# Optimization experiments

Measured on AMD Instinct MI355X. Metric: run time of the kernel, lower is better.

## Reference

```python
import jax, jax.numpy as jnp
import numpy as np

B, N = 8, 2048
IN_DIM, MEM_DIM, CTX_DIM = 256, 256, 128

def _linear_params(key, out_dim, in_dim):
    kw, kb = jax.random.split(key)
    bound = 1.0 / np.sqrt(in_dim)
    W = jax.random.uniform(kw, (out_dim, in_dim), jnp.float32, -bound, bound)
    b = jax.random.uniform(kb, (out_dim,), jnp.float32, -bound, bound)
    return W, b

def setup_inputs() -> dict:
    key = jax.random.key(0)
    ks = jax.random.split(key, 8)
    Wq, bq = _linear_params(ks[0], CTX_DIM, IN_DIM)
    Wk, bk = _linear_params(ks[1], CTX_DIM, MEM_DIM)
    Wv, bv = _linear_params(ks[2], MEM_DIM, MEM_DIM)
    Wu, bu = _linear_params(ks[3], MEM_DIM, IN_DIM + MEM_DIM)
    Wr, br = _linear_params(ks[4], MEM_DIM, IN_DIM + MEM_DIM)
    Wc, bc = _linear_params(ks[5], MEM_DIM, IN_DIM + MEM_DIM)
    input_tensor = jax.random.normal(ks[6], (B, N, IN_DIM), jnp.float32)
    previous_memory = jax.random.normal(ks[7], (B, N, MEM_DIM), jnp.float32)
    return dict(input_tensor=input_tensor, previous_memory=previous_memory,
                Wq=Wq, bq=bq, Wk=Wk, bk=bk, Wv=Wv, bv=bv,
                Wu=Wu, bu=bu, Wr=Wr, br=br, Wc=Wc, bc=bc)

def reference(input_tensor, previous_memory, Wq, bq, Wk, bk, Wv, bv, Wu, bu, Wr, br, Wc, bc):
    # QKV projections (torch Linear: y = x @ W.T + b)
    query = jnp.einsum('bnd,cd->bnc', input_tensor, Wq) + bq        # [B,N,CTX]
    key = jnp.einsum('bnm,cm->bnc', previous_memory, Wk) + bk       # [B,N,CTX]
    value = jnp.einsum('bnm,vm->bnv', previous_memory, Wv) + bv     # [B,N,MEM]
    attention_scores = jnp.einsum('bqc,bkc->bqk', query, key)        # [B,N,N]
    attention_probs = jax.nn.softmax(attention_scores, axis=-1)
    context_vector = jnp.einsum('bqk,bkv->bqv', attention_probs, value)  # computed but unused downstream, as in original
    combined = jnp.concatenate([input_tensor, previous_memory], axis=-1)  # [B,N,IN+MEM]
    update_gate = jax.nn.sigmoid(jnp.einsum('bnd,md->bnm', combined, Wu) + bu)
    reset_gate = jax.nn.sigmoid(jnp.einsum('bnd,md->bnm', combined, Wr) + br)
    cand_in = jnp.concatenate([input_tensor, reset_gate * previous_memory], axis=-1)
    candidate_memory = jnp.tanh(jnp.einsum('bnd,md->bnm', cand_in, Wc) + bc)
    new_memory = (1.0 - update_gate) * previous_memory + update_gate * candidate_memory
    return new_memory, attention_probs
```

## Files before the change

### kernel.cpp

```cpp
#include <hip/hip_runtime.h>


typedef _Float16 half8 __attribute__((ext_vector_type(8)));
typedef _Float16 half4 __attribute__((ext_vector_type(4)));
typedef float floatx4 __attribute__((ext_vector_type(4)));

#define MFMA16(a, b, c) __builtin_amdgcn_mfma_f32_16x16x32_f16((a), (b), (c), 0, 0, 0)

#define OFF_Q   524288
#define OFF_K   2621440

__device__ __forceinline__ void gload16(const void* g, void* l) {
  __builtin_amdgcn_global_load_lds((const __attribute__((address_space(1))) unsigned int*)g,
                                   (__attribute__((address_space(3))) unsigned int*)l, 16, 0, 0);
}

__global__ __launch_bounds__(512, 4) void kA(
    const float* __restrict__ input, const float* __restrict__ prev,
    const float* __restrict__ Wq, const float* __restrict__ bq,
    const float* __restrict__ Wk, const float* __restrict__ bk,
    const float* __restrict__ Wr, const float* __restrict__ br,
    const float* __restrict__ Wu, const float* __restrict__ bu,
    _Float16* __restrict__ ws,
    _Float16* __restrict__ t_sc, _Float16* __restrict__ u_sc)
{
  __shared__ char smem[32768];
  const int tid = threadIdx.x, w = tid >> 6, l = tid & 63;
  const int lr = l & 15, lg = l >> 4;

  if (blockIdx.x < 512) {
    const int b2 = blockIdx.x;
    const int rows0 = (b2 & 127) * 128;
    const int isU = w >> 2;
    const int c = (b2 >> 7) * 64 + (w & 3) * 16 + lr;

    const float* Wf = isU ? Wu : Wr;
    half8 bw[16];
#pragma unroll
    for (int ks = 0; ks < 16; ++ks) {
      floatx4 w0 = *(const floatx4*)(Wf + (size_t)c * 512 + ks * 32 + lg * 8);
      floatx4 w1 = *(const floatx4*)(Wf + (size_t)c * 512 + ks * 32 + lg * 8 + 4);
      half8 h;
#pragma unroll
      for (int j = 0; j < 4; ++j) { h[j] = (_Float16)w0[j]; h[4 + j] = (_Float16)w1[j]; }
      bw[ks] = h;
    }
    const float bv = (isU ? bu : br)[c];

    const int srow = tid >> 5, scol = (tid & 31) * 8;
    const int ssz = (srow & 7) << 4;
    floatx4 sI0, sI1, sP0, sP1;

#define K2RU_LOAD(ch) { \
  const float* si = input + ((size_t)rows0 + (ch) * 16 + srow) * 256 + scol; \
  const float* sp = prev  + ((size_t)rows0 + (ch) * 16 + srow) * 256 + scol; \
  sI0 = *(const floatx4*)si; sI1 = *(const floatx4*)(si + 4); \
  sP0 = *(const floatx4*)sp; sP1 = *(const floatx4*)(sp + 4); }
#define K2RU_WRITE(ch) { char* bufw = smem + ((ch) & 1) * 16384; \
  half8 hi, hp; \
  _Pragma("unroll") for (int j = 0; j < 4; ++j) { \
    hi[j] = (_Float16)sI0[j]; hi[4+j] = (_Float16)sI1[j]; \
    hp[j] = (_Float16)sP0[j]; hp[4+j] = (_Float16)sP1[j]; } \
  int o = srow * 1024 + ((scol * 2) ^ ssz); \
  *(half8*)(bufw + o) = hi; *(half8*)(bufw + o + 512) = hp; }

    K2RU_LOAD(0); K2RU_WRITE(0);
    __syncthreads();
#pragma unroll 1
    for (int ch = 0; ch < 8; ++ch) {
      if (ch < 7) K2RU_LOAD(ch + 1);
      const char* buf = smem + (ch & 1) * 16384;
      floatx4 acc = {0.f, 0.f, 0.f, 0.f};
      const int base = lr * 1024, sz = (lr & 7) << 4;
#pragma unroll
      for (int ks = 0; ks < 16; ++ks) {
        half8 a = *(const half8*)(buf + base + ((ks * 64 + lg * 16) ^ sz));
        acc = MFMA16(a, bw[ks], acc);
      }
#pragma unroll
      for (int j = 0; j < 4; ++j) {
        const int crow = lg * 4 + j;
        const size_t grow = (size_t)rows0 + ch * 16 + crow;
        float g = 1.f / (1.f + __expf(-(acc[j] + bv)));
        if (!isU) {
          float m = (float)*(const _Float16*)(buf + crow * 1024 + 512 + ((c * 2) ^ ((crow & 7) << 4)));
          t_sc[grow * 256 + c] = (_Float16)(g * m);
        } else {
          u_sc[grow * 256 + c] = (_Float16)g;
        }
      }
      if (ch < 7) K2RU_WRITE(ch + 1);
      __syncthreads();
    }
  } else {
    const int b1 = blockIdx.x - 512;
    const int which = b1 >> 8;
    const int rows0 = (b1 & 255) * 64;
    const float* x = which ? prev : input;
    const float* Wf = which ? Wk : Wq;
    const float* bias = which ? bk : bq;
    _Float16* out = ws + (which ? OFF_K : OFF_Q);
    const int c = w * 16 + lr;

    half8 bh[8], blo[8];
#pragma unroll
    for (int ks = 0; ks < 8; ++ks) {
      floatx4 w0 = *(const floatx4*)(Wf + (size_t)c * 256 + ks * 32 + lg * 8);
      floatx4 w1 = *(const floatx4*)(Wf + (size_t)c * 256 + ks * 32 + lg * 8 + 4);
      half8 h, lo;
#pragma unroll
      for (int j = 0; j < 4; ++j) {
        _Float16 h0 = (_Float16)w0[j];
        h[j] = h0; lo[j] = (_Float16)(w0[j] - (float)h0);
        _Float16 h1 = (_Float16)w1[j];
        h[4 + j] = h1; lo[4 + j] = (_Float16)(w1[j] - (float)h1);
      }
      bh[ks] = h; blo[ks] = lo;
    }
    const float bv = bias[c];

    const int srow = tid >> 5, scol = (tid & 31) * 8;
    const int ssz = (srow & 7) << 4;
    floatx4 st0, st1;

#define K1_LOAD(ch) { const float* src = x + ((size_t)rows0 + (ch) * 16 + srow) * 256 + scol; \
  st0 = *(const floatx4*)src; st1 = *(const floatx4*)(src + 4); }
#define K1_WRITE(ch) { char* bufw = smem + ((ch) & 1) * 8192; \
  half8 h; \
  _Pragma("unroll") for (int j = 0; j < 4; ++j) { \
    h[j] = (_Float16)st0[j]; h[4+j] = (_Float16)st1[j]; } \
  *(half8*)(bufw + srow * 512 + ((scol * 2) ^ ssz)) = h; }

    K1_LOAD(0); K1_WRITE(0);
    __syncthreads();
#pragma unroll 1
    for (int ch = 0; ch < 4; ++ch) {
      if (ch < 3) K1_LOAD(ch + 1);
      const char* buf = smem + (ch & 1) * 8192;
      floatx4 acc = {0.f, 0.f, 0.f, 0.f};
      const int base = lr * 512, sz = (lr & 7) << 4;
#pragma unroll
      for (int ks = 0; ks < 8; ++ks) {
        half8 ah = *(const half8*)(buf + base + ((ks * 64 + lg * 16) ^ sz));
        acc = MFMA16(ah, bh[ks], acc);
        acc = MFMA16(ah, blo[ks], acc);
      }
#pragma unroll
      for (int j = 0; j < 4; ++j)
        out[((size_t)rows0 + ch * 16 + lg * 4 + j) * 128 + c] = (_Float16)(acc[j] + bv);
      if (ch < 3) K1_WRITE(ch + 1);
      __syncthreads();
    }
  }
}

#define K3_STAGE(Kg, dst, ch) { \
  const char* g_ = (Kg) + (ch) * 32768; \
  _Pragma("unroll") for (int i_ = 0; i_ < 4; ++i_) { \
    int o_ = w * 1024 + i_ * 8192 + l * 16; \
    int row_ = o_ >> 8, col_ = o_ & 255; \
    gload16(g_ + row_ * 256 + (col_ ^ ((row_ & 7) << 4)), (dst) + w * 1024 + i_ * 8192); } }

__global__ __launch_bounds__(512, 4) void kB(
    const float* __restrict__ input, const float* __restrict__ prev,
    const float* __restrict__ Wc, const float* __restrict__ bc,
    const _Float16* __restrict__ ws, float* __restrict__ part,
    const _Float16* __restrict__ t_sc, const _Float16* __restrict__ u_sc,
    float* __restrict__ out0)
{
  __shared__ char smem[65536];
  const int tid = threadIdx.x, w = tid >> 6, l = tid & 63;
  const int lr = l & 15, lg = l >> 4;

  if (blockIdx.x < 512) {
    const int b3 = blockIdx.x;
    const int b = b3 & 7, q0 = ((b3 >> 3) & 15) * 128, kh = b3 >> 7;

    const _Float16* Q = ws + OFF_Q + ((size_t)b * 2048 + q0 + w * 16) * 128;
    const char* Kg = (const char*)(ws + OFF_K + ((size_t)b * 2048 + kh * 512) * 128);

    half8 qf[4];
#pragma unroll
    for (int ks = 0; ks < 4; ++ks)
      qf[ks] = *(const half8*)(Q + (size_t)lr * 128 + ks * 32 + lg * 8);

    char* kbuf0 = smem, * kbuf1 = smem + 32768;
    K3_STAGE(Kg, kbuf0, 0);
    __syncthreads();

    float se = 0.f;
#pragma unroll 1
    for (int ch = 0; ch < 4; ++ch) {
      if (ch < 3) K3_STAGE(Kg, ((ch + 1) & 1) ? kbuf1 : kbuf0, ch + 1);
      const char* buf = (ch & 1) ? kbuf1 : kbuf0;
#pragma unroll
      for (int kt = 0; kt < 8; ++kt) {
        const int kk = kt * 16 + lr;
        const int kbase = kk * 256, ksz = (kk & 7) << 4;
        half8 kf[4];
#pragma unroll
        for (int ks = 0; ks < 4; ++ks)
          kf[ks] = *(const half8*)(buf + kbase + ((ks * 64 + lg * 16) ^ ksz));
        floatx4 acc = {0.f, 0.f, 0.f, 0.f};
#pragma unroll
        for (int ks = 0; ks < 4; ++ks) acc = MFMA16(kf[ks], qf[ks], acc);
#pragma unroll
        for (int j = 0; j < 4; ++j) se += __expf(acc[j] - 14.f);
      }
      __syncthreads();
    }
    se += __shfl_xor(se, 16);
    se += __shfl_xor(se, 32);
    if (lg == 0)
      part[((size_t)b * 4 + kh) * 2048 + q0 + w * 16 + lr] = se;
  } else {
    const int b2 = blockIdx.x - 512;
    const int rows0 = (b2 & 255) * 64;
    const int c = (b2 >> 8) * 128 + w * 16 + lr;

    half8 bw[16];
#pragma unroll
    for (int ks = 0; ks < 16; ++ks) {
      floatx4 w0 = *(const floatx4*)(Wc + (size_t)c * 512 + ks * 32 + lg * 8);
      floatx4 w1 = *(const floatx4*)(Wc + (size_t)c * 512 + ks * 32 + lg * 8 + 4);
      half8 h;
#pragma unroll
      for (int j = 0; j < 4; ++j) { h[j] = (_Float16)w0[j]; h[4 + j] = (_Float16)w1[j]; }
      bw[ks] = h;
    }
    const float bv = bc[c];

    const int srow = tid >> 5, scol = (tid & 31) * 8;
    const int ssz = (srow & 7) << 4;
    floatx4 sI0, sI1;
    half8 sT;

#define K2C_LOAD(ch) { \
  const float* si = input + ((size_t)rows0 + (ch) * 16 + srow) * 256 + scol; \
  sI0 = *(const floatx4*)si; sI1 = *(const floatx4*)(si + 4); \
  sT = *(const half8*)(t_sc + ((size_t)rows0 + (ch) * 16 + srow) * 256 + scol); }
#define K2C_WRITE(ch) { char* bufw = smem + ((ch) & 1) * 16384; \
  half8 hi; \
  _Pragma("unroll") for (int j = 0; j < 4; ++j) { hi[j] = (_Float16)sI0[j]; hi[4+j] = (_Float16)sI1[j]; } \
  int o = srow * 1024 + ((scol * 2) ^ ssz); \
  *(half8*)(bufw + o) = hi; *(half8*)(bufw + o + 512) = sT; }

    K2C_LOAD(0); K2C_WRITE(0);
    __syncthreads();
#pragma unroll 1
    for (int ch = 0; ch < 4; ++ch) {
      if (ch < 3) K2C_LOAD(ch + 1);
      const char* buf = smem + (ch & 1) * 16384;
      floatx4 acc = {0.f, 0.f, 0.f, 0.f};
      const int base = lr * 1024, sz = (lr & 7) << 4;
#pragma unroll
      for (int ks = 0; ks < 16; ++ks) {
        half8 a = *(const half8*)(buf + base + ((ks * 64 + lg * 16) ^ sz));
        acc = MFMA16(a, bw[ks], acc);
      }
#pragma unroll
      for (int j = 0; j < 4; ++j) {
        const size_t grow = (size_t)rows0 + ch * 16 + lg * 4 + j;
        float e2 = __expf(2.f * (acc[j] + bv));
        float cg = (e2 - 1.f) / (e2 + 1.f);
        float u = (float)u_sc[grow * 256 + c];
        float m = prev[grow * 256 + c];
        out0[grow * 256 + c] = (1.f - u) * m + u * cg;
      }
      if (ch < 3) K2C_WRITE(ch + 1);
      __syncthreads();
    }
  }
}

__global__ __launch_bounds__(512) void k3b_store(
    const _Float16* __restrict__ ws, const float* __restrict__ part,
    float* __restrict__ out1)
{
  __shared__ char kbuf[2][32768];
  const int b = blockIdx.x, q0 = blockIdx.y * 128, kh = blockIdx.z;
  const int tid = threadIdx.x, w = tid >> 6, l = tid & 63;
  const int lr = l & 15, lg = l >> 4;

  const int q = q0 + w * 16 + lr;
  const _Float16* Q = ws + OFF_Q + ((size_t)b * 2048 + q0 + w * 16) * 128;
  const char* Kg = (const char*)(ws + OFF_K + ((size_t)b * 2048 + kh * 512) * 128);

  half8 qf[4];
#pragma unroll
  for (int ks = 0; ks < 4; ++ks)
    qf[ks] = *(const half8*)(Q + (size_t)lr * 128 + ks * 32 + lg * 8);
  const float inv = 1.f / (part[(size_t)(b * 4 + 0) * 2048 + q] +
                           part[(size_t)(b * 4 + 1) * 2048 + q] +
                           part[(size_t)(b * 4 + 2) * 2048 + q] +
                           part[(size_t)(b * 4 + 3) * 2048 + q]);

  K3_STAGE(Kg, kbuf[0], 0);
  __syncthreads();

  float* orow = out1 + ((size_t)b * 2048 + q) * 2048 + kh * 512;
#pragma unroll 1
  for (int ch = 0; ch < 4; ++ch) {
    if (ch < 3) K3_STAGE(Kg, kbuf[(ch + 1) & 1], ch + 1);
    const char* buf = kbuf[ch & 1];
#pragma unroll
    for (int kt = 0; kt < 8; ++kt) {
      const int kk = kt * 16 + lr;
      const int kbase = kk * 256, ksz = (kk & 7) << 4;
      half8 kf[4];
#pragma unroll
      for (int ks = 0; ks < 4; ++ks)
        kf[ks] = *(const half8*)(buf + kbase + ((ks * 64 + lg * 16) ^ ksz));
      floatx4 acc = {0.f, 0.f, 0.f, 0.f};
#pragma unroll
      for (int ks = 0; ks < 4; ++ks) acc = MFMA16(kf[ks], qf[ks], acc);
      floatx4 v;
#pragma unroll
      for (int j = 0; j < 4; ++j) v[j] = __expf(acc[j] - 14.f) * inv;
      *(floatx4*)(orow + ch * 128 + kt * 16 + lg * 4) = v;
    }
    __syncthreads();
  }
}

extern "C" void kernel_launch(void* const* d_in, const int* in_sizes, int n_in,
                              void* d_out, int out_size, void* d_ws, size_t ws_size,
                              hipStream_t stream)
{
  const float* input = (const float*)d_in[0];
  const float* prev  = (const float*)d_in[1];
  const float* Wq = (const float*)d_in[2];
  const float* bq = (const float*)d_in[3];
  const float* Wk = (const float*)d_in[4];
  const float* bk = (const float*)d_in[5];
  const float* Wu = (const float*)d_in[8];
  const float* bu = (const float*)d_in[9];
  const float* Wr = (const float*)d_in[10];
  const float* br = (const float*)d_in[11];
  const float* Wc = (const float*)d_in[12];
  const float* bc = (const float*)d_in[13];

  float* out0 = (float*)d_out;
  float* out1 = out0 + (size_t)8 * 2048 * 256;
  _Float16* ws = (_Float16*)d_ws;

  _Float16* t_sc = (_Float16*)out1;
  _Float16* u_sc = (_Float16*)out1 + 4194304;
  float* part = (float*)ws;

  hipLaunchKernelGGL(kA, dim3(1024), dim3(512), 0, stream,
                     input, prev, Wq, bq, Wk, bk, Wr, br, Wu, bu, ws, t_sc, u_sc);
  hipLaunchKernelGGL(kB, dim3(1024), dim3(512), 0, stream,
                     input, prev, Wc, bc, ws, part, t_sc, u_sc, out0);
  hipLaunchKernelGGL(k3b_store, dim3(8, 16, 4), dim3(512), 0, stream, ws, part, out1);
}
```

Before: 110.3 us.

## Fuse three kernels into one cooperative persistent kernel with grid barriers

Moves each former kernel's work into a device role function and runs all of them from one cooperative kernel of 512 blocks. Each block runs two roles in sequence (gates plus QK projection, then softmax sums plus candidate update, then the probability store), and grid.sync separates the phases. The aim is to cut kernel launch and tail gaps between the three launches. In exchange each block does serial work, grid barriers add their own cost, and an occupancy query runs on every call; the old three-kernel path is kept as a fallback when fewer than two blocks fit per CU.

```diff
diff --git a/kernel.cpp b/kernel.cpp
--- a/kernel.cpp
+++ b/kernel.cpp
@@ -1,4 +1,7 @@
 #include <hip/hip_runtime.h>
+#include <hip/hip_cooperative_groups.h>
+
+namespace cg = cooperative_groups;
 
 
 typedef _Float16 half8 __attribute__((ext_vector_type(8)));
@@ -15,41 +18,36 @@
                                    (__attribute__((address_space(3))) unsigned int*)l, 16, 0, 0);
 }
 
-__global__ __launch_bounds__(512, 4) void kA(
-    const float* __restrict__ input, const float* __restrict__ prev,
-    const float* __restrict__ Wq, const float* __restrict__ bq,
-    const float* __restrict__ Wk, const float* __restrict__ bk,
+
+__device__ __forceinline__ void role_k2ru(
+    char* smem, int job, int tid,
+    const float* __restrict__ input, const float* __restrict__ prev,
     const float* __restrict__ Wr, const float* __restrict__ br,
     const float* __restrict__ Wu, const float* __restrict__ bu,
-    _Float16* __restrict__ ws,
     _Float16* __restrict__ t_sc, _Float16* __restrict__ u_sc)
 {
-  __shared__ char smem[32768];
-  const int tid = threadIdx.x, w = tid >> 6, l = tid & 63;
+  const int w = tid >> 6, l = tid & 63;
   const int lr = l & 15, lg = l >> 4;
-
-  if (blockIdx.x < 512) {
-    const int b2 = blockIdx.x;
-    const int rows0 = (b2 & 127) * 128;
-    const int isU = w >> 2;
-    const int c = (b2 >> 7) * 64 + (w & 3) * 16 + lr;
-
-    const float* Wf = isU ? Wu : Wr;
-    half8 bw[16];
-#pragma unroll
-    for (int ks = 0; ks < 16; ++ks) {
-      floatx4 w0 = *(const floatx4*)(Wf + (size_t)c * 512 + ks * 32 + lg * 8);
-      floatx4 w1 = *(const floatx4*)(Wf + (size_t)c * 512 + ks * 32 + lg * 8 + 4);
-      half8 h;
-#pragma unroll
-      for (int j = 0; j < 4; ++j) { h[j] = (_Float16)w0[j]; h[4 + j] = (_Float16)w1[j]; }
-      bw[ks] = h;
-    }
-    const float bv = (isU ? bu : br)[c];
-
-    const int srow = tid >> 5, scol = (tid & 31) * 8;
-    const int ssz = (srow & 7) << 4;
-    floatx4 sI0, sI1, sP0, sP1;
+  const int rows0 = (job & 127) * 128;
+  const int isU = w >> 2;
+  const int c = (job >> 7) * 64 + (w & 3) * 16 + lr;
+
+  const float* Wf = isU ? Wu : Wr;
+  half8 bw[16];
+#pragma unroll
+  for (int ks = 0; ks < 16; ++ks) {
+    floatx4 w0 = *(const floatx4*)(Wf + (size_t)c * 512 + ks * 32 + lg * 8);
+    floatx4 w1 = *(const floatx4*)(Wf + (size_t)c * 512 + ks * 32 + lg * 8 + 4);
+    half8 h;
+#pragma unroll
+    for (int j = 0; j < 4; ++j) { h[j] = (_Float16)w0[j]; h[4 + j] = (_Float16)w1[j]; }
+    bw[ks] = h;
+  }
+  const float bv = (isU ? bu : br)[c];
+
+  const int srow = tid >> 5, scol = (tid & 31) * 8;
+  const int ssz = (srow & 7) << 4;
+  floatx4 sI0, sI1, sP0, sP1;
 
 #define K2RU_LOAD(ch) { \
   const float* si = input + ((size_t)rows0 + (ch) * 16 + srow) * 256 + scol; \
@@ -64,64 +62,73 @@
   int o = srow * 1024 + ((scol * 2) ^ ssz); \
   *(half8*)(bufw + o) = hi; *(half8*)(bufw + o + 512) = hp; }
 
-    K2RU_LOAD(0); K2RU_WRITE(0);
+  K2RU_LOAD(0); K2RU_WRITE(0);
+  __syncthreads();
+#pragma unroll 1
+  for (int ch = 0; ch < 8; ++ch) {
+    if (ch < 7) K2RU_LOAD(ch + 1);
+    const char* buf = smem + (ch & 1) * 16384;
+    floatx4 acc = {0.f, 0.f, 0.f, 0.f};
+    const int base = lr * 1024, sz = (lr & 7) << 4;
+#pragma unroll
+    for (int ks = 0; ks < 16; ++ks) {
+      half8 a = *(const half8*)(buf + base + ((ks * 64 + lg * 16) ^ sz));
+      acc = MFMA16(a, bw[ks], acc);
+    }
+#pragma unroll
+    for (int j = 0; j < 4; ++j) {
+      const int crow = lg * 4 + j;
+      const size_t grow = (size_t)rows0 + ch * 16 + crow;
+      float g = 1.f / (1.f + __expf(-(acc[j] + bv)));
+      if (!isU) {
+        float m = (float)*(const _Float16*)(buf + crow * 1024 + 512 + ((c * 2) ^ ((crow & 7) << 4)));
+        t_sc[grow * 256 + c] = (_Float16)(g * m);
+      } else {
+        u_sc[grow * 256 + c] = (_Float16)g;
+      }
+    }
+    if (ch < 7) K2RU_WRITE(ch + 1);
     __syncthreads();
-#pragma unroll 1
-    for (int ch = 0; ch < 8; ++ch) {
-      if (ch < 7) K2RU_LOAD(ch + 1);
-      const char* buf = smem + (ch & 1) * 16384;
-      floatx4 acc = {0.f, 0.f, 0.f, 0.f};
-      const int base = lr * 1024, sz = (lr & 7) << 4;
-#pragma unroll
-      for (int ks = 0; ks < 16; ++ks) {
-        half8 a = *(const half8*)(buf + base + ((ks * 64 + lg * 16) ^ sz));
-        acc = MFMA16(a, bw[ks], acc);
-      }
-#pragma unroll
-      for (int j = 0; j < 4; ++j) {
-        const int crow = lg * 4 + j;
-        const size_t grow = (size_t)rows0 + ch * 16 + crow;
-        float g = 1.f / (1.f + __expf(-(acc[j] + bv)));
-        if (!isU) {
-          float m = (float)*(const _Float16*)(buf + crow * 1024 + 512 + ((c * 2) ^ ((crow & 7) << 4)));
-          t_sc[grow * 256 + c] = (_Float16)(g * m);
-        } else {
-          u_sc[grow * 256 + c] = (_Float16)g;
-        }
-      }
-      if (ch < 7) K2RU_WRITE(ch + 1);
-      __syncthreads();
-    }
-  } else {
-    const int b1 = blockIdx.x - 512;
-    const int which = b1 >> 8;
-    const int rows0 = (b1 & 255) * 64;
-    const float* x = which ? prev : input;
-    const float* Wf = which ? Wk : Wq;
-    const float* bias = which ? bk : bq;
-    _Float16* out = ws + (which ? OFF_K : OFF_Q);
-    const int c = w * 16 + lr;
-
-    half8 bh[8], blo[8];
-#pragma unroll
-    for (int ks = 0; ks < 8; ++ks) {
-      floatx4 w0 = *(const floatx4*)(Wf + (size_t)c * 256 + ks * 32 + lg * 8);
-      floatx4 w1 = *(const floatx4*)(Wf + (size_t)c * 256 + ks * 32 + lg * 8 + 4);
-      half8 h, lo;
-#pragma unroll
-      for (int j = 0; j < 4; ++j) {
-        _Float16 h0 = (_Float16)w0[j];
-        h[j] = h0; lo[j] = (_Float16)(w0[j] - (float)h0);
-        _Float16 h1 = (_Float16)w1[j];
-        h[4 + j] = h1; lo[4 + j] = (_Float16)(w1[j] - (float)h1);
-      }
-      bh[ks] = h; blo[ks] = lo;
-    }
-    const float bv = bias[c];
-
-    const int srow = tid >> 5, scol = (tid & 31) * 8;
-    const int ssz = (srow & 7) << 4;
-    floatx4 st0, st1;
+  }
+}
+
+__device__ __forceinline__ void role_k1(
+    char* smem, int job, int tid,
+    const float* __restrict__ input, const float* __restrict__ prev,
+    const float* __restrict__ Wq, const float* __restrict__ bq,
+    const float* __restrict__ Wk, const float* __restrict__ bk,
+    _Float16* __restrict__ ws)
+{
+  const int w = tid >> 6, l = tid & 63;
+  const int lr = l & 15, lg = l >> 4;
+  const int which = job >> 8;
+  const int rows0 = (job & 255) * 64;
+  const float* x = which ? prev : input;
+  const float* Wf = which ? Wk : Wq;
+  const float* bias = which ? bk : bq;
+  _Float16* out = ws + (which ? OFF_K : OFF_Q);
+  const int c = w * 16 + lr;
+
+  half8 bh[8], blo[8];
+#pragma unroll
+  for (int ks = 0; ks < 8; ++ks) {
+    floatx4 w0 = *(const floatx4*)(Wf + (size_t)c * 256 + ks * 32 + lg * 8);
+    floatx4 w1 = *(const floatx4*)(Wf + (size_t)c * 256 + ks * 32 + lg * 8 + 4);
+    half8 h, lo;
+#pragma unroll
+    for (int j = 0; j < 4; ++j) {
+      _Float16 h0 = (_Float16)w0[j];
+      h[j] = h0; lo[j] = (_Float16)(w0[j] - (float)h0);
+      _Float16 h1 = (_Float16)w1[j];
+      h[4 + j] = h1; lo[4 + j] = (_Float16)(w1[j] - (float)h1);
+    }
+    bh[ks] = h; blo[ks] = lo;
+  }
+  const float bv = bias[c];
+
+  const int srow = tid >> 5, scol = (tid & 31) * 8;
+  const int ssz = (srow & 7) << 4;
+  floatx4 st0, st1;
 
 #define K1_LOAD(ch) { const float* src = x + ((size_t)rows0 + (ch) * 16 + srow) * 256 + scol; \
   st0 = *(const floatx4*)src; st1 = *(const floatx4*)(src + 4); }
@@ -131,26 +138,25 @@
     h[j] = (_Float16)st0[j]; h[4+j] = (_Float16)st1[j]; } \
   *(half8*)(bufw + srow * 512 + ((scol * 2) ^ ssz)) = h; }
 
-    K1_LOAD(0); K1_WRITE(0);
+  K1_LOAD(0); K1_WRITE(0);
+  __syncthreads();
+#pragma unroll 1
+  for (int ch = 0; ch < 4; ++ch) {
+    if (ch < 3) K1_LOAD(ch + 1);
+    const char* buf = smem + (ch & 1) * 8192;
+    floatx4 acc = {0.f, 0.f, 0.f, 0.f};
+    const int base = lr * 512, sz = (lr & 7) << 4;
+#pragma unroll
+    for (int ks = 0; ks < 8; ++ks) {
+      half8 ah = *(const half8*)(buf + base + ((ks * 64 + lg * 16) ^ sz));
+      acc = MFMA16(ah, bh[ks], acc);
+      acc = MFMA16(ah, blo[ks], acc);
+    }
+#pragma unroll
+    for (int j = 0; j < 4; ++j)
+      out[((size_t)rows0 + ch * 16 + lg * 4 + j) * 128 + c] = (_Float16)(acc[j] + bv);
+    if (ch < 3) K1_WRITE(ch + 1);
     __syncthreads();
-#pragma unroll 1
-    for (int ch = 0; ch < 4; ++ch) {
-      if (ch < 3) K1_LOAD(ch + 1);
-      const char* buf = smem + (ch & 1) * 8192;
-      floatx4 acc = {0.f, 0.f, 0.f, 0.f};
-      const int base = lr * 512, sz = (lr & 7) << 4;
-#pragma unroll
-      for (int ks = 0; ks < 8; ++ks) {
-        half8 ah = *(const half8*)(buf + base + ((ks * 64 + lg * 16) ^ sz));
-        acc = MFMA16(ah, bh[ks], acc);
-        acc = MFMA16(ah, blo[ks], acc);
-      }
-#pragma unroll
-      for (int j = 0; j < 4; ++j)
-        out[((size_t)rows0 + ch * 16 + lg * 4 + j) * 128 + c] = (_Float16)(acc[j] + bv);
-      if (ch < 3) K1_WRITE(ch + 1);
-      __syncthreads();
-    }
   }
 }
 
@@ -161,79 +167,81 @@
     int row_ = o_ >> 8, col_ = o_ & 255; \
     gload16(g_ + row_ * 256 + (col_ ^ ((row_ & 7) << 4)), (dst) + w * 1024 + i_ * 8192); } }
 
-__global__ __launch_bounds__(512, 4) void kB(
+__device__ __forceinline__ void role_k3a(
+    char* smem, int job, int tid,
+    const _Float16* __restrict__ ws, float* __restrict__ part)
+{
+  const int w = tid >> 6, l = tid & 63;
+  const int lr = l & 15, lg = l >> 4;
+  const int b = job & 7, q0 = ((job >> 3) & 15) * 128, kh = job >> 7;
+
+  const _Float16* Q = ws + OFF_Q + ((size_t)b * 2048 + q0 + w * 16) * 128;
+  const char* Kg = (const char*)(ws + OFF_K + ((size_t)b * 2048 + kh * 512) * 128);
+
+  half8 qf[4];
+#pragma unroll
+  for (int ks = 0; ks < 4; ++ks)
+    qf[ks] = *(const half8*)(Q + (size_t)lr * 128 + ks * 32 + lg * 8);
+
+  char* kbuf0 = smem; char* kbuf1 = smem + 32768;
+  K3_STAGE(Kg, kbuf0, 0);
+  __syncthreads();
+
+  float se = 0.f;
+#pragma unroll 1
+  for (int ch = 0; ch < 4; ++ch) {
+    if (ch < 3) K3_STAGE(Kg, ((ch + 1) & 1) ? kbuf1 : kbuf0, ch + 1);
+    const char* buf = (ch & 1) ? kbuf1 : kbuf0;
+#pragma unroll
+    for (int kt = 0; kt < 8; ++kt) {
+      const int kk = kt * 16 + lr;
+      const int kbase = kk * 256, ksz = (kk & 7) << 4;
+      half8 kf[4];
+#pragma unroll
+      for (int ks = 0; ks < 4; ++ks)
+        kf[ks] = *(const half8*)(buf + kbase + ((ks * 64 + lg * 16) ^ ksz));
+      floatx4 acc = {0.f, 0.f, 0.f, 0.f};
+#pragma unroll
+      for (int ks = 0; ks < 4; ++ks) acc = MFMA16(kf[ks], qf[ks], acc);
+#pragma unroll
+      for (int j = 0; j < 4; ++j) se += __expf(acc[j] - 14.f);
+    }
+    __syncthreads();
+  }
+  se += __shfl_xor(se, 16);
+  se += __shfl_xor(se, 32);
+  if (lg == 0)
+    part[((size_t)b * 4 + kh) * 2048 + q0 + w * 16 + lr] = se;
+}
+
+__device__ __forceinline__ void role_k2c(
+    char* smem, int job, int tid,
     const float* __restrict__ input, const float* __restrict__ prev,
     const float* __restrict__ Wc, const float* __restrict__ bc,
-    const _Float16* __restrict__ ws, float* __restrict__ part,
     const _Float16* __restrict__ t_sc, const _Float16* __restrict__ u_sc,
     float* __restrict__ out0)
 {
-  __shared__ char smem[65536];
-  const int tid = threadIdx.x, w = tid >> 6, l = tid & 63;
+  const int w = tid >> 6, l = tid & 63;
   const int lr = l & 15, lg = l >> 4;
-
-  if (blockIdx.x < 512) {
-    const int b3 = blockIdx.x;
-    const int b = b3 & 7, q0 = ((b3 >> 3) & 15) * 128, kh = b3 >> 7;
-
-    const _Float16* Q = ws + OFF_Q + ((size_t)b * 2048 + q0 + w * 16) * 128;
-    const char* Kg = (const char*)(ws + OFF_K + ((size_t)b * 2048 + kh * 512) * 128);
-
-    half8 qf[4];
-#pragma unroll
-    for (int ks = 0; ks < 4; ++ks)
-      qf[ks] = *(const half8*)(Q + (size_t)lr * 128 + ks * 32 + lg * 8);
-
-    char* kbuf0 = smem, * kbuf1 = smem + 32768;
-    K3_STAGE(Kg, kbuf0, 0);
-    __syncthreads();
-
-    float se = 0.f;
-#pragma unroll 1
-    for (int ch = 0; ch < 4; ++ch) {
-      if (ch < 3) K3_STAGE(Kg, ((ch + 1) & 1) ? kbuf1 : kbuf0, ch + 1);
-      const char* buf = (ch & 1) ? kbuf1 : kbuf0;
-#pragma unroll
-      for (int kt = 0; kt < 8; ++kt) {
-        const int kk = kt * 16 + lr;
-        const int kbase = kk * 256, ksz = (kk & 7) << 4;
-        half8 kf[4];
-#pragma unroll
-        for (int ks = 0; ks < 4; ++ks)
-          kf[ks] = *(const half8*)(buf + kbase + ((ks * 64 + lg * 16) ^ ksz));
-        floatx4 acc = {0.f, 0.f, 0.f, 0.f};
-#pragma unroll
-        for (int ks = 0; ks < 4; ++ks) acc = MFMA16(kf[ks], qf[ks], acc);
-#pragma unroll
-        for (int j = 0; j < 4; ++j) se += __expf(acc[j] - 14.f);
-      }
-      __syncthreads();
-    }
-    se += __shfl_xor(se, 16);
-    se += __shfl_xor(se, 32);
-    if (lg == 0)
-      part[((size_t)b * 4 + kh) * 2048 + q0 + w * 16 + lr] = se;
-  } else {
-    const int b2 = blockIdx.x - 512;
-    const int rows0 = (b2 & 255) * 64;
-    const int c = (b2 >> 8) * 128 + w * 16 + lr;
-
-    half8 bw[16];
-#pragma unroll
-    for (int ks = 0; ks < 16; ++ks) {
-      floatx4 w0 = *(const floatx4*)(Wc + (size_t)c * 512 + ks * 32 + lg * 8);
-      floatx4 w1 = *(const floatx4*)(Wc + (size_t)c * 512 + ks * 32 + lg * 8 + 4);
-      half8 h;
-#pragma unroll
-      for (int j = 0; j < 4; ++j) { h[j] = (_Float16)w0[j]; h[4 + j] = (_Float16)w1[j]; }
-      bw[ks] = h;
-    }
-    const float bv = bc[c];
-
-    const int srow = tid >> 5, scol = (tid & 31) * 8;
-    const int ssz = (srow & 7) << 4;
-    floatx4 sI0, sI1;
-    half8 sT;
+  const int rows0 = (job & 255) * 64;
+  const int c = (job >> 8) * 128 + w * 16 + lr;
+
+  half8 bw[16];
+#pragma unroll
+  for (int ks = 0; ks < 16; ++ks) {
+    floatx4 w0 = *(const floatx4*)(Wc + (size_t)c * 512 + ks * 32 + lg * 8);
+    floatx4 w1 = *(const floatx4*)(Wc + (size_t)c * 512 + ks * 32 + lg * 8 + 4);
+    half8 h;
+#pragma unroll
+    for (int j = 0; j < 4; ++j) { h[j] = (_Float16)w0[j]; h[4 + j] = (_Float16)w1[j]; }
+    bw[ks] = h;
+  }
+  const float bv = bc[c];
+
+  const int srow = tid >> 5, scol = (tid & 31) * 8;
+  const int ssz = (srow & 7) << 4;
+  floatx4 sI0, sI1;
+  half8 sT;
 
 #define K2C_LOAD(ch) { \
   const float* si = input + ((size_t)rows0 + (ch) * 16 + srow) * 256 + scol; \
@@ -245,42 +253,41 @@
   int o = srow * 1024 + ((scol * 2) ^ ssz); \
   *(half8*)(bufw + o) = hi; *(half8*)(bufw + o + 512) = sT; }
 
-    K2C_LOAD(0); K2C_WRITE(0);
+  K2C_LOAD(0); K2C_WRITE(0);
+  __syncthreads();
+#pragma unroll 1
+  for (int ch = 0; ch < 4; ++ch) {
+    if (ch < 3) K2C_LOAD(ch + 1);
+    const char* buf = smem + (ch & 1) * 16384;
+    floatx4 acc = {0.f, 0.f, 0.f, 0.f};
+    const int base = lr * 1024, sz = (lr & 7) << 4;
+#pragma unroll
+    for (int ks = 0; ks < 16; ++ks) {
+      half8 a = *(const half8*)(buf + base + ((ks * 64 + lg * 16) ^ sz));
+      acc = MFMA16(a, bw[ks], acc);
+    }
+#pragma unroll
+    for (int j = 0; j < 4; ++j) {
+      const size_t grow = (size_t)rows0 + ch * 16 + lg * 4 + j;
+      float e2 = __expf(2.f * (acc[j] + bv));
+      float cg = (e2 - 1.f) / (e2 + 1.f);
+      float u = (float)u_sc[grow * 256 + c];
+      float m = prev[grow * 256 + c];
+      out0[grow * 256 + c] = (1.f - u) * m + u * cg;
+    }
+    if (ch < 3) K2C_WRITE(ch + 1);
     __syncthreads();
-#pragma unroll 1
-    for (int ch = 0; ch < 4; ++ch) {
-      if (ch < 3) K2C_LOAD(ch + 1);
-      const char* buf = smem + (ch & 1) * 16384;
-      floatx4 acc = {0.f, 0.f, 0.f, 0.f};
-      const int base = lr * 1024, sz = (lr & 7) << 4;
-#pragma unroll
-      for (int ks = 0; ks < 16; ++ks) {
-        half8 a = *(const half8*)(buf + base + ((ks * 64 + lg * 16) ^ sz));
-        acc = MFMA16(a, bw[ks], acc);
-      }
-#pragma unroll
-      for (int j = 0; j < 4; ++j) {
-        const size_t grow = (size_t)rows0 + ch * 16 + lg * 4 + j;
-        float e2 = __expf(2.f * (acc[j] + bv));
-        float cg = (e2 - 1.f) / (e2 + 1.f);
-        float u = (float)u_sc[grow * 256 + c];
-        float m = prev[grow * 256 + c];
-        out0[grow * 256 + c] = (1.f - u) * m + u * cg;
-      }
-      if (ch < 3) K2C_WRITE(ch + 1);
-      __syncthreads();
-    }
-  }
-}
-
-__global__ __launch_bounds__(512) void k3b_store(
+  }
+}
+
+__device__ __forceinline__ void role_k3b(
+    char* smem, int job, int tid,
     const _Float16* __restrict__ ws, const float* __restrict__ part,
     float* __restrict__ out1)
 {
-  __shared__ char kbuf[2][32768];
-  const int b = blockIdx.x, q0 = blockIdx.y * 128, kh = blockIdx.z;
-  const int tid = threadIdx.x, w = tid >> 6, l = tid & 63;
+  const int w = tid >> 6, l = tid & 63;
   const int lr = l & 15, lg = l >> 4;
+  const int b = job & 7, q0 = ((job >> 3) & 15) * 128, kh = job >> 7;
 
   const int q = q0 + w * 16 + lr;
   const _Float16* Q = ws + OFF_Q + ((size_t)b * 2048 + q0 + w * 16) * 128;
@@ -295,14 +302,15 @@
                            part[(size_t)(b * 4 + 2) * 2048 + q] +
                            part[(size_t)(b * 4 + 3) * 2048 + q]);
 
-  K3_STAGE(Kg, kbuf[0], 0);
+  char* kbuf0 = smem; char* kbuf1 = smem + 32768;
+  K3_STAGE(Kg, kbuf0, 0);
   __syncthreads();
 
   float* orow = out1 + ((size_t)b * 2048 + q) * 2048 + kh * 512;
 #pragma unroll 1
   for (int ch = 0; ch < 4; ++ch) {
-    if (ch < 3) K3_STAGE(Kg, kbuf[(ch + 1) & 1], ch + 1);
-    const char* buf = kbuf[ch & 1];
+    if (ch < 3) K3_STAGE(Kg, ((ch + 1) & 1) ? kbuf1 : kbuf0, ch + 1);
+    const char* buf = (ch & 1) ? kbuf1 : kbuf0;
 #pragma unroll
     for (int kt = 0; kt < 8; ++kt) {
       const int kk = kt * 16 + lr;
@@ -321,6 +329,72 @@
     }
     __syncthreads();
   }
+}
+
+__global__ __launch_bounds__(512, 4) void mega(
+    const float* __restrict__ input, const float* __restrict__ prev,
+    const float* __restrict__ Wq, const float* __restrict__ bq,
+    const float* __restrict__ Wk, const float* __restrict__ bk,
+    const float* __restrict__ Wr, const float* __restrict__ br,
+    const float* __restrict__ Wu, const float* __restrict__ bu,
+    const float* __restrict__ Wc, const float* __restrict__ bc,
+    _Float16* __restrict__ ws, float* __restrict__ part,
+    _Float16* __restrict__ t_sc, _Float16* __restrict__ u_sc,
+    float* __restrict__ out0, float* __restrict__ out1)
+{
+  __shared__ char smem[65536];
+  cg::grid_group grid = cg::this_grid();
+  const int bid = blockIdx.x, tid = threadIdx.x;
+
+  role_k2ru(smem, bid, tid, input, prev, Wr, br, Wu, bu, t_sc, u_sc);
+  __syncthreads();
+  role_k1(smem, bid, tid, input, prev, Wq, bq, Wk, bk, ws);
+  grid.sync();
+
+  role_k3a(smem, bid, tid, ws, part);
+  __syncthreads();
+  role_k2c(smem, bid, tid, input, prev, Wc, bc, t_sc, u_sc, out0);
+  grid.sync();
+
+  role_k3b(smem, bid, tid, ws, part, out1);
+}
+
+__global__ __launch_bounds__(512, 4) void kA_fb(
+    const float* __restrict__ input, const float* __restrict__ prev,
+    const float* __restrict__ Wq, const float* __restrict__ bq,
+    const float* __restrict__ Wk, const float* __restrict__ bk,
+    const float* __restrict__ Wr, const float* __restrict__ br,
+    const float* __restrict__ Wu, const float* __restrict__ bu,
+    _Float16* __restrict__ ws,
+    _Float16* __restrict__ t_sc, _Float16* __restrict__ u_sc)
+{
+  __shared__ char smem[32768];
+  if (blockIdx.x < 512)
+    role_k2ru(smem, blockIdx.x, threadIdx.x, input, prev, Wr, br, Wu, bu, t_sc, u_sc);
+  else
+    role_k1(smem, blockIdx.x - 512, threadIdx.x, input, prev, Wq, bq, Wk, bk, ws);
+}
+
+__global__ __launch_bounds__(512, 4) void kB_fb(
+    const float* __restrict__ input, const float* __restrict__ prev,
+    const float* __restrict__ Wc, const float* __restrict__ bc,
+    const _Float16* __restrict__ ws, float* __restrict__ part,
+    const _Float16* __restrict__ t_sc, const _Float16* __restrict__ u_sc,
+    float* __restrict__ out0)
+{
+  __shared__ char smem[65536];
+  if (blockIdx.x < 512)
+    role_k3a(smem, blockIdx.x, threadIdx.x, ws, part);
+  else
+    role_k2c(smem, blockIdx.x - 512, threadIdx.x, input, prev, Wc, bc, t_sc, u_sc, out0);
+}
+
+__global__ __launch_bounds__(512, 4) void kC_fb(
+    const _Float16* __restrict__ ws, const float* __restrict__ part,
+    float* __restrict__ out1)
+{
+  __shared__ char smem[65536];
+  role_k3b(smem, blockIdx.x, threadIdx.x, ws, part, out1);
 }
 
 extern "C" void kernel_launch(void* const* d_in, const int* in_sizes, int n_in,
@@ -348,9 +422,21 @@
   _Float16* u_sc = (_Float16*)out1 + 4194304;
   float* part = (float*)ws;
 
-  hipLaunchKernelGGL(kA, dim3(1024), dim3(512), 0, stream,
-                     input, prev, Wq, bq, Wk, bk, Wr, br, Wu, bu, ws, t_sc, u_sc);
-  hipLaunchKernelGGL(kB, dim3(1024), dim3(512), 0, stream,
-                     input, prev, Wc, bc, ws, part, t_sc, u_sc, out0);
-  hipLaunchKernelGGL(k3b_store, dim3(8, 16, 4), dim3(512), 0, stream, ws, part, out1);
-}
+  int occ = 0;
+  hipOccupancyMaxActiveBlocksPerMultiprocessor(&occ, (const void*)mega, 512, 0);
+
+  if (occ >= 2) {
+    void* args[] = { (void*)&input, (void*)&prev, (void*)&Wq, (void*)&bq,
+                     (void*)&Wk, (void*)&bk, (void*)&Wr, (void*)&br,
+                     (void*)&Wu, (void*)&bu, (void*)&Wc, (void*)&bc,
+                     (void*)&ws, (void*)&part, (void*)&t_sc, (void*)&u_sc,
+                     (void*)&out0, (void*)&out1 };
+    hipLaunchCooperativeKernel((void*)mega, dim3(512), dim3(512), args, 0, stream);
+  } else {
+    hipLaunchKernelGGL(kA_fb, dim3(1024), dim3(512), 0, stream,
+                       input, prev, Wq, bq, Wk, bk, Wr, br, Wu, bu, ws, t_sc, u_sc);
+    hipLaunchKernelGGL(kB_fb, dim3(1024), dim3(512), 0, stream,
+                       input, prev, Wc, bc, ws, part, t_sc, u_sc, out0);
+    hipLaunchKernelGGL(kC_fb, dim3(512), dim3(512), 0, stream, ws, part, out1);
+  }
+}
```

After: 111.0 us. About the same (+0.6%).

## Halve block size to 256 threads and double grid across all three kernels

Applied to the files above, without the earlier changes.

Every kernel now runs 256-thread blocks with twice as many blocks. Each block covers half the output columns (gates, Q/K projections, candidate) or half the query rows (attention). The staging loads are reshaped so each thread moves 16 elements per row instead of 8. The K-chunk size in the attention kernels is halved, which halves shared memory per block and doubles the number of pipeline steps. The aim is better occupancy and load balance across CUs, at the cost of more per-block weight loading and more synchronisation steps.

```diff
diff --git a/kernel.cpp b/kernel.cpp
--- a/kernel.cpp
+++ b/kernel.cpp
@@ -2,7 +2,6 @@
 
 
 typedef _Float16 half8 __attribute__((ext_vector_type(8)));
-typedef _Float16 half4 __attribute__((ext_vector_type(4)));
 typedef float floatx4 __attribute__((ext_vector_type(4)));
 
 #define MFMA16(a, b, c) __builtin_amdgcn_mfma_f32_16x16x32_f16((a), (b), (c), 0, 0, 0)
@@ -15,7 +14,7 @@
                                    (__attribute__((address_space(3))) unsigned int*)l, 16, 0, 0);
 }
 
-__global__ __launch_bounds__(512, 4) void kA(
+__global__ __launch_bounds__(256, 4) void kA(
     const float* __restrict__ input, const float* __restrict__ prev,
     const float* __restrict__ Wq, const float* __restrict__ bq,
     const float* __restrict__ Wk, const float* __restrict__ bk,
@@ -28,11 +27,11 @@
   const int tid = threadIdx.x, w = tid >> 6, l = tid & 63;
   const int lr = l & 15, lg = l >> 4;
 
-  if (blockIdx.x < 512) {
-    const int b2 = blockIdx.x;
-    const int rows0 = (b2 & 127) * 128;
-    const int isU = w >> 2;
-    const int c = (b2 >> 7) * 64 + (w & 3) * 16 + lr;
+  if (blockIdx.x < 1024) {
+    const int job = blockIdx.x;
+    const int rows0 = (job & 127) * 128;
+    const int isU = w >> 1;
+    const int c = (job >> 7) * 32 + (w & 1) * 16 + lr;
 
     const float* Wf = isU ? Wu : Wr;
     half8 bw[16];
@@ -47,22 +46,28 @@
     }
     const float bv = (isU ? bu : br)[c];
 
-    const int srow = tid >> 5, scol = (tid & 31) * 8;
+    const int srow = tid >> 4, spart = tid & 15;
     const int ssz = (srow & 7) << 4;
-    floatx4 sI0, sI1, sP0, sP1;
+    floatx4 a0, a1, a2, a3, p0, p1, p2, p3;
 
 #define K2RU_LOAD(ch) { \
-  const float* si = input + ((size_t)rows0 + (ch) * 16 + srow) * 256 + scol; \
-  const float* sp = prev  + ((size_t)rows0 + (ch) * 16 + srow) * 256 + scol; \
-  sI0 = *(const floatx4*)si; sI1 = *(const floatx4*)(si + 4); \
-  sP0 = *(const floatx4*)sp; sP1 = *(const floatx4*)(sp + 4); }
+  const float* si = input + ((size_t)rows0 + (ch) * 16 + srow) * 256 + spart * 16; \
+  const float* sp = prev  + ((size_t)rows0 + (ch) * 16 + srow) * 256 + spart * 16; \
+  a0 = *(const floatx4*)si;       a1 = *(const floatx4*)(si + 4); \
+  a2 = *(const floatx4*)(si + 8); a3 = *(const floatx4*)(si + 12); \
+  p0 = *(const floatx4*)sp;       p1 = *(const floatx4*)(sp + 4); \
+  p2 = *(const floatx4*)(sp + 8); p3 = *(const floatx4*)(sp + 12); }
 #define K2RU_WRITE(ch) { char* bufw = smem + ((ch) & 1) * 16384; \
-  half8 hi, hp; \
+  half8 h0, h1, q0h, q1h; \
   _Pragma("unroll") for (int j = 0; j < 4; ++j) { \
-    hi[j] = (_Float16)sI0[j]; hi[4+j] = (_Float16)sI1[j]; \
-    hp[j] = (_Float16)sP0[j]; hp[4+j] = (_Float16)sP1[j]; } \
-  int o = srow * 1024 + ((scol * 2) ^ ssz); \
-  *(half8*)(bufw + o) = hi; *(half8*)(bufw + o + 512) = hp; }
+    h0[j] = (_Float16)a0[j]; h0[4+j] = (_Float16)a1[j]; \
+    h1[j] = (_Float16)a2[j]; h1[4+j] = (_Float16)a3[j]; \
+    q0h[j] = (_Float16)p0[j]; q0h[4+j] = (_Float16)p1[j]; \
+    q1h[j] = (_Float16)p2[j]; q1h[4+j] = (_Float16)p3[j]; } \
+  int o0 = srow * 1024 + ((spart * 32) ^ ssz); \
+  int o1 = srow * 1024 + ((spart * 32 + 16) ^ ssz); \
+  *(half8*)(bufw + o0) = h0;       *(half8*)(bufw + o1) = h1; \
+  *(half8*)(bufw + o0 + 512) = q0h; *(half8*)(bufw + o1 + 512) = q1h; }
 
     K2RU_LOAD(0); K2RU_WRITE(0);
     __syncthreads();
@@ -93,14 +98,15 @@
       __syncthreads();
     }
   } else {
-    const int b1 = blockIdx.x - 512;
-    const int which = b1 >> 8;
-    const int rows0 = (b1 & 255) * 64;
+    const int job = blockIdx.x - 1024;
+    const int which = job >> 9;
+    const int rem = job & 511;
+    const int rows0 = (rem >> 1) * 64;
     const float* x = which ? prev : input;
     const float* Wf = which ? Wk : Wq;
     const float* bias = which ? bk : bq;
     _Float16* out = ws + (which ? OFF_K : OFF_Q);
-    const int c = w * 16 + lr;
+    const int c = (rem & 1) * 64 + w * 16 + lr;
 
     half8 bh[8], blo[8];
 #pragma unroll
@@ -119,17 +125,22 @@
     }
     const float bv = bias[c];
 
-    const int srow = tid >> 5, scol = (tid & 31) * 8;
+    const int srow = tid >> 4, spart = tid & 15;
     const int ssz = (srow & 7) << 4;
-    floatx4 st0, st1;
-
-#define K1_LOAD(ch) { const float* src = x + ((size_t)rows0 + (ch) * 16 + srow) * 256 + scol; \
-  st0 = *(const floatx4*)src; st1 = *(const floatx4*)(src + 4); }
+    floatx4 a0, a1, a2, a3;
+
+#define K1_LOAD(ch) { \
+  const float* src = x + ((size_t)rows0 + (ch) * 16 + srow) * 256 + spart * 16; \
+  a0 = *(const floatx4*)src;       a1 = *(const floatx4*)(src + 4); \
+  a2 = *(const floatx4*)(src + 8); a3 = *(const floatx4*)(src + 12); }
 #define K1_WRITE(ch) { char* bufw = smem + ((ch) & 1) * 8192; \
-  half8 h; \
+  half8 h0, h1; \
   _Pragma("unroll") for (int j = 0; j < 4; ++j) { \
-    h[j] = (_Float16)st0[j]; h[4+j] = (_Float16)st1[j]; } \
-  *(half8*)(bufw + srow * 512 + ((scol * 2) ^ ssz)) = h; }
+    h0[j] = (_Float16)a0[j]; h0[4+j] = (_Float16)a1[j]; \
+    h1[j] = (_Float16)a2[j]; h1[4+j] = (_Float16)a3[j]; } \
+  int o0 = srow * 512 + ((spart * 32) ^ ssz); \
+  int o1 = srow * 512 + ((spart * 32 + 16) ^ ssz); \
+  *(half8*)(bufw + o0) = h0; *(half8*)(bufw + o1) = h1; }
 
     K1_LOAD(0); K1_WRITE(0);
     __syncthreads();
@@ -155,26 +166,26 @@
 }
 
 #define K3_STAGE(Kg, dst, ch) { \
-  const char* g_ = (Kg) + (ch) * 32768; \
+  const char* g_ = (Kg) + (ch) * 16384; \
   _Pragma("unroll") for (int i_ = 0; i_ < 4; ++i_) { \
-    int o_ = w * 1024 + i_ * 8192 + l * 16; \
+    int o_ = i_ * 4096 + w * 1024 + l * 16; \
     int row_ = o_ >> 8, col_ = o_ & 255; \
-    gload16(g_ + row_ * 256 + (col_ ^ ((row_ & 7) << 4)), (dst) + w * 1024 + i_ * 8192); } }
-
-__global__ __launch_bounds__(512, 4) void kB(
+    gload16(g_ + row_ * 256 + (col_ ^ ((row_ & 7) << 4)), (dst) + o_); } }
+
+__global__ __launch_bounds__(256, 4) void kB(
     const float* __restrict__ input, const float* __restrict__ prev,
     const float* __restrict__ Wc, const float* __restrict__ bc,
     const _Float16* __restrict__ ws, float* __restrict__ part,
     const _Float16* __restrict__ t_sc, const _Float16* __restrict__ u_sc,
     float* __restrict__ out0)
 {
-  __shared__ char smem[65536];
+  __shared__ char smem[32768];
   const int tid = threadIdx.x, w = tid >> 6, l = tid & 63;
   const int lr = l & 15, lg = l >> 4;
 
-  if (blockIdx.x < 512) {
-    const int b3 = blockIdx.x;
-    const int b = b3 & 7, q0 = ((b3 >> 3) & 15) * 128, kh = b3 >> 7;
+  if (blockIdx.x < 1024) {
+    const int job = blockIdx.x;
+    const int b = job & 7, q0 = ((job >> 3) & 31) * 64, kh = job >> 8;
 
     const _Float16* Q = ws + OFF_Q + ((size_t)b * 2048 + q0 + w * 16) * 128;
     const char* Kg = (const char*)(ws + OFF_K + ((size_t)b * 2048 + kh * 512) * 128);
@@ -184,17 +195,17 @@
     for (int ks = 0; ks < 4; ++ks)
       qf[ks] = *(const half8*)(Q + (size_t)lr * 128 + ks * 32 + lg * 8);
 
-    char* kbuf0 = smem, * kbuf1 = smem + 32768;
+    char* kbuf0 = smem; char* kbuf1 = smem + 16384;
     K3_STAGE(Kg, kbuf0, 0);
     __syncthreads();
 
     float se = 0.f;
 #pragma unroll 1
-    for (int ch = 0; ch < 4; ++ch) {
-      if (ch < 3) K3_STAGE(Kg, ((ch + 1) & 1) ? kbuf1 : kbuf0, ch + 1);
+    for (int ch = 0; ch < 8; ++ch) {
+      if (ch < 7) K3_STAGE(Kg, ((ch + 1) & 1) ? kbuf1 : kbuf0, ch + 1);
       const char* buf = (ch & 1) ? kbuf1 : kbuf0;
 #pragma unroll
-      for (int kt = 0; kt < 8; ++kt) {
+      for (int kt = 0; kt < 4; ++kt) {
         const int kk = kt * 16 + lr;
         const int kbase = kk * 256, ksz = (kk & 7) << 4;
         half8 kf[4];
@@ -214,9 +225,9 @@
     if (lg == 0)
       part[((size_t)b * 4 + kh) * 2048 + q0 + w * 16 + lr] = se;
   } else {
-    const int b2 = blockIdx.x - 512;
-    const int rows0 = (b2 & 255) * 64;
-    const int c = (b2 >> 8) * 128 + w * 16 + lr;
+    const int job = blockIdx.x - 1024;
+    const int rows0 = (job & 255) * 64;
+    const int c = (job >> 8) * 64 + w * 16 + lr;
 
     half8 bw[16];
 #pragma unroll
@@ -230,20 +241,26 @@
     }
     const float bv = bc[c];
 
-    const int srow = tid >> 5, scol = (tid & 31) * 8;
+    const int srow = tid >> 4, spart = tid & 15;
     const int ssz = (srow & 7) << 4;
-    floatx4 sI0, sI1;
-    half8 sT;
+    floatx4 a0, a1, a2, a3;
+    half8 t0, t1;
 
 #define K2C_LOAD(ch) { \
-  const float* si = input + ((size_t)rows0 + (ch) * 16 + srow) * 256 + scol; \
-  sI0 = *(const floatx4*)si; sI1 = *(const floatx4*)(si + 4); \
-  sT = *(const half8*)(t_sc + ((size_t)rows0 + (ch) * 16 + srow) * 256 + scol); }
+  const float* si = input + ((size_t)rows0 + (ch) * 16 + srow) * 256 + spart * 16; \
+  const _Float16* stp = t_sc + ((size_t)rows0 + (ch) * 16 + srow) * 256 + spart * 16; \
+  a0 = *(const floatx4*)si;       a1 = *(const floatx4*)(si + 4); \
+  a2 = *(const floatx4*)(si + 8); a3 = *(const floatx4*)(si + 12); \
+  t0 = *(const half8*)stp; t1 = *(const half8*)(stp + 8); }
 #define K2C_WRITE(ch) { char* bufw = smem + ((ch) & 1) * 16384; \
-  half8 hi; \
-  _Pragma("unroll") for (int j = 0; j < 4; ++j) { hi[j] = (_Float16)sI0[j]; hi[4+j] = (_Float16)sI1[j]; } \
-  int o = srow * 1024 + ((scol * 2) ^ ssz); \
-  *(half8*)(bufw + o) = hi; *(half8*)(bufw + o + 512) = sT; }
+  half8 h0, h1; \
+  _Pragma("unroll") for (int j = 0; j < 4; ++j) { \
+    h0[j] = (_Float16)a0[j]; h0[4+j] = (_Float16)a1[j]; \
+    h1[j] = (_Float16)a2[j]; h1[4+j] = (_Float16)a3[j]; } \
+  int o0 = srow * 1024 + ((spart * 32) ^ ssz); \
+  int o1 = srow * 1024 + ((spart * 32 + 16) ^ ssz); \
+  *(half8*)(bufw + o0) = h0;      *(half8*)(bufw + o1) = h1; \
+  *(half8*)(bufw + o0 + 512) = t0; *(half8*)(bufw + o1 + 512) = t1; }
 
     K2C_LOAD(0); K2C_WRITE(0);
     __syncthreads();
@@ -273,14 +290,15 @@
   }
 }
 
-__global__ __launch_bounds__(512) void k3b_store(
+__global__ __launch_bounds__(256, 4) void kC(
     const _Float16* __restrict__ ws, const float* __restrict__ part,
     float* __restrict__ out1)
 {
-  __shared__ char kbuf[2][32768];
-  const int b = blockIdx.x, q0 = blockIdx.y * 128, kh = blockIdx.z;
+  __shared__ char smem[32768];
   const int tid = threadIdx.x, w = tid >> 6, l = tid & 63;
   const int lr = l & 15, lg = l >> 4;
+  const int job = blockIdx.x;
+  const int b = job & 7, q0 = ((job >> 3) & 31) * 64, kh = job >> 8;
 
   const int q = q0 + w * 16 + lr;
   const _Float16* Q = ws + OFF_Q + ((size_t)b * 2048 + q0 + w * 16) * 128;
@@ -295,16 +313,17 @@
                            part[(size_t)(b * 4 + 2) * 2048 + q] +
                            part[(size_t)(b * 4 + 3) * 2048 + q]);
 
-  K3_STAGE(Kg, kbuf[0], 0);
+  char* kbuf0 = smem; char* kbuf1 = smem + 16384;
+  K3_STAGE(Kg, kbuf0, 0);
   __syncthreads();
 
   float* orow = out1 + ((size_t)b * 2048 + q) * 2048 + kh * 512;
 #pragma unroll 1
-  for (int ch = 0; ch < 4; ++ch) {
-    if (ch < 3) K3_STAGE(Kg, kbuf[(ch + 1) & 1], ch + 1);
-    const char* buf = kbuf[ch & 1];
-#pragma unroll
-    for (int kt = 0; kt < 8; ++kt) {
+  for (int ch = 0; ch < 8; ++ch) {
+    if (ch < 7) K3_STAGE(Kg, ((ch + 1) & 1) ? kbuf1 : kbuf0, ch + 1);
+    const char* buf = (ch & 1) ? kbuf1 : kbuf0;
+#pragma unroll
+    for (int kt = 0; kt < 4; ++kt) {
       const int kk = kt * 16 + lr;
       const int kbase = kk * 256, ksz = (kk & 7) << 4;
       half8 kf[4];
@@ -317,7 +336,7 @@
       floatx4 v;
 #pragma unroll
       for (int j = 0; j < 4; ++j) v[j] = __expf(acc[j] - 14.f) * inv;
-      *(floatx4*)(orow + ch * 128 + kt * 16 + lg * 4) = v;
+      *(floatx4*)(orow + ch * 64 + kt * 16 + lg * 4) = v;
     }
     __syncthreads();
   }
@@ -348,9 +367,9 @@
   _Float16* u_sc = (_Float16*)out1 + 4194304;
   float* part = (float*)ws;
 
-  hipLaunchKernelGGL(kA, dim3(1024), dim3(512), 0, stream,
+  hipLaunchKernelGGL(kA, dim3(2048), dim3(256), 0, stream,
                      input, prev, Wq, bq, Wk, bk, Wr, br, Wu, bu, ws, t_sc, u_sc);
-  hipLaunchKernelGGL(kB, dim3(1024), dim3(512), 0, stream,
+  hipLaunchKernelGGL(kB, dim3(2048), dim3(256), 0, stream,
                      input, prev, Wc, bc, ws, part, t_sc, u_sc, out0);
-  hipLaunchKernelGGL(k3b_store, dim3(8, 16, 4), dim3(512), 0, stream, ws, part, out1);
-}
+  hipLaunchKernelGGL(kC, dim3(1024), dim3(256), 0, stream, ws, part, out1);
+}
```

Result: slower. 142.4 us (+29.1%).
